# Performance work log

Measured on AMD Instinct MI355X. Metric: run time of the kernel, lower is better.

The kernel has to match this reference:

```python
import jax, jax.numpy as jnp
import numpy as np
from jax import lax

EPS = 1e-5
COMMIT_W = 0.25

def conv2d(x, w, b):
    # x: [N,C,H,W], w: [O,I,3,3], SAME padding, stride 1
    y = lax.conv_general_dilated(x, w, (1, 1), 'SAME',
                                 dimension_numbers=('NCHW', 'OIHW', 'NCHW'))
    return y + b[None, :, None, None]

def batchnorm(x, gamma, beta):
    # training-mode batch norm over (N,H,W)
    m = jnp.mean(x, axis=(0, 2, 3), keepdims=True)
    v = jnp.var(x, axis=(0, 2, 3), keepdims=True)
    xhat = (x - m) * lax.rsqrt(v + EPS)
    return xhat * gamma[None, :, None, None] + beta[None, :, None, None]

def maxpool2(x):
    return lax.reduce_window(x, -jnp.inf, lax.max, (1, 1, 2, 2), (1, 1, 2, 2), 'VALID')

def setup_inputs() -> dict:
    key = jax.random.key(0)
    ks = jax.random.split(key, 8)
    B, C, H, W, D, K = 8, 3, 256, 256, 64, 1024
    return {
        'x': jax.random.normal(ks[0], (B, C, H, W), jnp.float32),
        'conv1_w': jax.random.normal(ks[1], (D, C, 3, 3), jnp.float32) * 0.05,
        'conv1_b': jnp.zeros((D,), jnp.float32),
        'bn1_gamma': jnp.ones((D,), jnp.float32),
        'bn1_beta': jnp.zeros((D,), jnp.float32),
        'embed': jax.random.normal(ks[2], (K, D), jnp.float32),
        'conv2_w': jax.random.normal(ks[3], (C, D, 3, 3), jnp.float32) * 0.05,
        'conv2_b': jnp.zeros((C,), jnp.float32),
        'bn2_gamma': jnp.ones((C,), jnp.float32),
        'bn2_beta': jnp.zeros((C,), jnp.float32),
    }

def reference(x, conv1_w, conv1_b, bn1_gamma, bn1_beta, embed,
              conv2_w, conv2_b, bn2_gamma, bn2_beta):
    # ---- encoder ----
    h = conv2d(x, conv1_w, conv1_b)
    h = batchnorm(h, bn1_gamma, bn1_beta)
    h = jax.nn.relu(h)
    h = maxpool2(h)                      # [B, D, H/2, W/2]
    B, D, Hh, Wh = h.shape
    # ---- vector quantize (accept_image_fmap) ----
    flat = jnp.transpose(h, (0, 2, 3, 1)).reshape(-1, D)   # [N, D]
    # squared euclidean distance to each code
    dist = (jnp.sum(flat * flat, axis=1, keepdims=True)
            - 2.0 * flat @ embed.T
            + jnp.sum(embed * embed, axis=1)[None, :])     # [N, K]
    idx = jnp.argmin(dist, axis=1)                          # [N]
    quant = embed[idx]                                      # gather [N, D]
    commit_loss = COMMIT_W * jnp.mean((lax.stop_gradient(quant) - flat) ** 2)
    # straight-through estimator
    quant_st = flat + lax.stop_gradient(quant - flat)
    q = jnp.transpose(quant_st.reshape(B, Hh, Wh, D), (0, 3, 1, 2))  # [B,D,Hh,Wh]
    indices = idx.reshape(B, Hh, Wh)
    # ---- decoder ----
    up = jnp.repeat(jnp.repeat(q, 2, axis=2), 2, axis=3)    # nearest x2
    y = conv2d(up, conv2_w, conv2_b)
    y = batchnorm(y, bn2_gamma, bn2_beta)
    y = jnp.tanh(y)
    return (y, indices, commit_loss)
```

## Files before the change

### kernel.cpp

```cpp
#include <hip/hip_runtime.h>
#include <hip/hip_bf16.h>
#include <math.h>

typedef unsigned int u32;
typedef unsigned short u16;
typedef __attribute__((ext_vector_type(8))) short short8v;
typedef __attribute__((ext_vector_type(4))) float f32x4;

#define HH 256
#define WW 256
#define HP 128
#define WP 128
#define NPTS (8*HP*WP)
#define NPIX 524288
#define Y_ELEMS (8*3*HH*WW)
#define IDX_OFF Y_ELEMS
#define LOSS_OFF (Y_ELEMS + NPTS)
#define MARGIN_MFMA 0.05f

__device__ __forceinline__ u32 bfr(float f) {
  u32 u = __float_as_uint(f);
  return (u + 0x7FFFu + ((u >> 16) & 1u)) >> 16;
}
__device__ __forceinline__ float bff(u32 h) { return __uint_as_float(h << 16); }

__global__ __launch_bounds__(256) void k1_fused(
    const float* __restrict__ x, const float* __restrict__ w1,
    const float* __restrict__ b1, double* __restrict__ part1,
    float* __restrict__ pooled) {
  __shared__ float wl[27*64];
  __shared__ float b1s[64];
  __shared__ float xs[3][4][68];
  __shared__ double sred[4][128];
  int t = threadIdx.x;
  for (int i = t; i < 27*64; i += 256) { int c = i & 63; int tap = i >> 6; wl[i] = w1[c*27 + tap]; }
  if (t < 64) b1s[t] = b1[t];
  int bx = blockIdx.x;
  int b = bx >> 9;
  int pid0 = (bx & 511) * 32;
  int py = pid0 >> 7;
  int px0 = pid0 & 127;
  int gcol0 = 2*px0 - 1, grow0 = 2*py - 1;
  for (int i = t; i < 816; i += 256) {
    int j = i % 68;
    int rr = (i / 68) & 3;
    int ic = i / 272;
    int col = gcol0 + j, row = grow0 + rr;
    float v = 0.f;
    if (col >= 0 && col < WW && row >= 0 && row < HH)
      v = x[((size_t)((b*3 + ic)*HH + row))*WW + col];
    xs[ic][rr][j] = v;
  }
  __syncthreads();
  int lpx = t >> 3;
  int co = (t & 7) * 8;
  float A0[8], A1[8], C0[8], C1[8];
  #pragma unroll
  for (int c = 0; c < 8; ++c) { float bb = b1s[co + c]; A0[c] = bb; A1[c] = bb; C0[c] = bb; C1[c] = bb; }
  #pragma unroll
  for (int ic = 0; ic < 3; ++ic) {
    #pragma unroll
    for (int dy = 0; dy < 3; ++dy) {
      const float* wb = wl + (size_t)((ic*3 + dy)*3)*64 + co;
      int j0 = 2*lpx;
      float xa0 = xs[ic][dy][j0+0], xa1 = xs[ic][dy][j0+1], xa2 = xs[ic][dy][j0+2], xa3 = xs[ic][dy][j0+3];
      float xc0 = xs[ic][dy+1][j0+0], xc1 = xs[ic][dy+1][j0+1], xc2 = xs[ic][dy+1][j0+2], xc3 = xs[ic][dy+1][j0+3];
      #pragma unroll
      for (int c = 0; c < 8; ++c) {
        float w0 = wb[c], w1v = wb[64 + c], w2v = wb[128 + c];
        A0[c] = fmaf(xa0, w0, fmaf(xa1, w1v, fmaf(xa2, w2v, A0[c])));
        A1[c] = fmaf(xa1, w0, fmaf(xa2, w1v, fmaf(xa3, w2v, A1[c])));
        C0[c] = fmaf(xc0, w0, fmaf(xc1, w1v, fmaf(xc2, w2v, C0[c])));
        C1[c] = fmaf(xc1, w0, fmaf(xc2, w1v, fmaf(xc3, w2v, C1[c])));
      }
    }
  }
  double s[8], q[8];
  float m[8];
  #pragma unroll
  for (int c = 0; c < 8; ++c) {
    double dA0 = (double)A0[c], dA1 = (double)A1[c], dC0 = (double)C0[c], dC1 = (double)C1[c];
    double s_ = 0.0;
    s_ += dA0 + dA1;
    double q_ = fma(dA0, dA0, 0.0);
    q_ = fma(dA1, dA1, q_);
    float m_ = fmaxf(-3.4e38f, fmaxf(A0[c], A1[c]));
    s_ += dC0 + dC1;
    q_ = fma(dC0, dC0, q_);
    q_ = fma(dC1, dC1, q_);
    m_ = fmaxf(m_, fmaxf(C0[c], C1[c]));
    s[c] = s_; q[c] = q_; m[c] = m_;
  }
  int pid = pid0 + lpx;
  size_t p = (size_t)b*16384 + pid;
  *(float4*)(pooled + p*64 + co)     = make_float4(m[0], m[1], m[2], m[3]);
  *(float4*)(pooled + p*64 + co + 4) = make_float4(m[4], m[5], m[6], m[7]);
  #pragma unroll 1
  for (int c = 0; c < 8; ++c) {
    #pragma unroll
    for (int st = 8; st < 64; st <<= 1) {
      s[c] += __shfl_xor(s[c], st, 64);
      q[c] += __shfl_xor(q[c], st, 64);
    }
  }
  int w = t >> 6;
  if ((t & 63) < 8) {
    #pragma unroll
    for (int c = 0; c < 8; ++c) {
      sred[w][co + c] = s[c];
      sred[w][64 + co + c] = q[c];
    }
  }
  __syncthreads();
  if (t < 128)
    part1[(size_t)bx*128 + t] = (sred[0][t] + sred[1][t]) + (sred[2][t] + sred[3][t]);
}

__global__ __launch_bounds__(256) void k2_reduce_bn1(
    const double* __restrict__ part1, const float* __restrict__ gamma,
    const float* __restrict__ beta, double* __restrict__ sAB1) {
  int c = blockIdx.x, t = threadIdx.x;
  double s = 0.0, q = 0.0;
  for (int i = t; i < 4096; i += 256) {
    const double* p = part1 + (size_t)i*128;
    s += p[c];
    q += p[64 + c];
  }
  __shared__ double ls[256], lq[256];
  ls[t] = s; lq[t] = q;
  __syncthreads();
  for (int o = 128; o > 0; o >>= 1) {
    if (t < o) { ls[t] += ls[t+o]; lq[t] += lq[t+o]; }
    __syncthreads();
  }
  if (t == 0) {
    double mean = ls[0] / (double)NPIX;
    double var  = lq[0] / (double)NPIX - mean*mean;
    double A = (double)gamma[c] / sqrt(var + 1e-5);
    sAB1[c] = A;
    sAB1[64 + c] = (double)beta[c] - mean*A;
  }
}

__global__ void kE_prep(const float* __restrict__ embed, char* __restrict__ epack,
                        double* __restrict__ enormd, float* __restrict__ enf,
                        u32* __restrict__ flagcnt,
                        const float* __restrict__ w2, float* __restrict__ weff) {
  int bxx = blockIdx.x;
  if (bxx >= 4) {
    int e = (bxx - 4)*256 + threadIdx.x;
    if (e >= 16*64*4) return;
    int oc = e & 3;
    int ic = (e >> 2) & 63;
    int combo = e >> 8;
    if (oc == 3) { weff[e] = 0.f; return; }
    int bq = combo & 1, a = (combo >> 1) & 1, ex = (combo >> 2) & 1, ey = combo >> 3;
    int rs = (a == 0) ? 0 : (ey == 0 ? 1 : 2);
    int rc = ((a ^ ey) != 0) ? 2 : 1;
    int cs = (bq == 0) ? 0 : (ex == 0 ? 1 : 2);
    int cc = ((bq ^ ex) != 0) ? 2 : 1;
    float ssum = 0.f;
    for (int i = 0; i < rc; ++i)
      for (int j = 0; j < cc; ++j)
        ssum += w2[((oc*64 + ic)*3 + (rs + i))*3 + (cs + j)];
    weff[e] = ssum;
    return;
  }
  if (bxx == 0 && threadIdx.x == 0) flagcnt[0] = 0u;
  int k = bxx*256 + threadIdx.x;
  const float4* e4 = (const float4*)(embed + (size_t)k*64);
  u32 hw[32], lw[32];
  double s0 = 0.0, s1 = 0.0;
  #pragma unroll
  for (int i = 0; i < 16; ++i) {
    float4 v = e4[i];
    float f0 = v.x, f1 = v.y, f2 = v.z, f3 = v.w;
    s0 = fma((double)f0, (double)f0, s0); s1 = fma((double)f1, (double)f1, s1);
    s0 = fma((double)f2, (double)f2, s0); s1 = fma((double)f3, (double)f3, s1);
    u32 h0 = bfr(f0), h1 = bfr(f1), h2 = bfr(f2), h3 = bfr(f3);
    u32 l0 = bfr(f0 - bff(h0)), l1 = bfr(f1 - bff(h1));
    u32 l2 = bfr(f2 - bff(h2)), l3 = bfr(f3 - bff(h3));
    hw[2*i]   = h0 | (h1 << 16);
    hw[2*i+1] = h2 | (h3 << 16);
    lw[2*i]   = l0 | (l1 << 16);
    lw[2*i+1] = l2 | (l3 << 16);
  }
  char* tb = epack + (size_t)(k >> 4)*4096 + (size_t)(k & 15)*16;
  #pragma unroll
  for (int g = 0; g < 4; ++g) {
    *(uint4*)(tb + 0*1024 + g*256) = make_uint4(hw[4*g+0], hw[4*g+1], hw[4*g+2], hw[4*g+3]);
    *(uint4*)(tb + 1*1024 + g*256) = make_uint4(hw[16+4*g+0], hw[16+4*g+1], hw[16+4*g+2], hw[16+4*g+3]);
    *(uint4*)(tb + 2*1024 + g*256) = make_uint4(lw[4*g+0], lw[4*g+1], lw[4*g+2], lw[4*g+3]);
    *(uint4*)(tb + 3*1024 + g*256) = make_uint4(lw[16+4*g+0], lw[16+4*g+1], lw[16+4*g+2], lw[16+4*g+3]);
  }
  double e = s0 + s1;
  enormd[k] = e;
  enf[k] = (float)e;
}

#define MFMA_BF16 __builtin_amdgcn_mfma_f32_16x16x32_bf16
#define PROC_T(ntv) { \
  int code = (ntv)*16 + col; \
  float en2 = senf[code];    \
  f32x4 accA0={en2,en2,en2,en2}, accA1={0.f,0.f,0.f,0.f}; \
  f32x4 accB0={en2,en2,en2,en2}, accB1={0.f,0.f,0.f,0.f}; \
  accA0 = MFMA_BF16(aA_h0, b_h0, accA0, 0, 0, 0); \
  accA1 = MFMA_BF16(aA_h1, b_h1, accA1, 0, 0, 0); \
  accB0 = MFMA_BF16(aB_h0, b_h0, accB0, 0, 0, 0); \
  accB1 = MFMA_BF16(aB_h1, b_h1, accB1, 0, 0, 0); \
  accA0 = MFMA_BF16(aA_l0, b_h0, accA0, 0, 0, 0); \
  accA1 = MFMA_BF16(aA_l1, b_h1, accA1, 0, 0, 0); \
  accB0 = MFMA_BF16(aB_l0, b_h0, accB0, 0, 0, 0); \
  accB1 = MFMA_BF16(aB_l1, b_h1, accB1, 0, 0, 0); \
  accA0 = MFMA_BF16(aA_h0, b_l0, accA0, 0, 0, 0); \
  accA1 = MFMA_BF16(aA_h1, b_l1, accA1, 0, 0, 0); \
  accB0 = MFMA_BF16(aB_h0, b_l0, accB0, 0, 0, 0); \
  accB1 = MFMA_BF16(aB_h1, b_l1, accB1, 0, 0, 0); \
  _Pragma("unroll") \
  for (int j = 0; j < 4; ++j) { \
    float mA = accA0[j] + accA1[j]; \
    bool cA = mA > bestA[j]; \
    b2A[j] = fmaxf(b2A[j], fminf(mA, bestA[j])); \
    bestA[j] = fmaxf(bestA[j], mA); \
    idxA[j] = cA ? code : idxA[j]; \
    float mB = accB0[j] + accB1[j]; \
    bool cB = mB > bestB[j]; \
    b2B[j] = fmaxf(b2B[j], fminf(mB, bestB[j])); \
    bestB[j] = fmaxf(bestB[j], mB); \
    idxB[j] = cB ? code : idxB[j]; \
  } \
}
#define PROC_LDS(bb, ntv) { \
  short8v b_h0 = *(const short8v*)((bb) + 0*1024 + lane*16); \
  short8v b_h1 = *(const short8v*)((bb) + 1*1024 + lane*16); \
  short8v b_l0 = *(const short8v*)((bb) + 2*1024 + lane*16); \
  short8v b_l1 = *(const short8v*)((bb) + 3*1024 + lane*16); \
  PROC_T(ntv); \
}

__global__ __launch_bounds__(256) void kB_mfma(
    const float* __restrict__ pooled, const double* __restrict__ sAB1,
    const char* __restrict__ epack, const float* __restrict__ enf,
    int* __restrict__ idxbuf, float* __restrict__ out_f, double* __restrict__ lossq,
    u32* __restrict__ flagcnt, u32* __restrict__ flagids) {
  __shared__ float senf[1024];
  __shared__ char shbuf[32768];
  __shared__ float fnp[256];
  __shared__ float fnsum[128];
  __shared__ float sAs[64], sBs[64];
  __shared__ double wred[4];
  int t = threadIdx.x;
  for (int i = t; i < 1024; i += 256) senf[i] = -0.5f * enf[i];
  if (t < 64) { sAs[t] = (float)sAB1[t]; sBs[t] = (float)sAB1[64 + t]; }
  __syncthreads();
  {
    int lp = t >> 1, h = t & 1, cb = h*32;
    int p = blockIdx.x*128 + lp;
    const float4* src = (const float4*)(pooled + (size_t)p*64 + cb);
    float fn = 0.f;
    u32 hw[16], lw[16];
    #pragma unroll
    for (int i = 0; i < 8; ++i) {
      float4 v = src[i];
      float f0 = fmaxf(fmaf(v.x, sAs[cb+4*i+0], sBs[cb+4*i+0]), 0.f);
      float f1 = fmaxf(fmaf(v.y, sAs[cb+4*i+1], sBs[cb+4*i+1]), 0.f);
      float f2 = fmaxf(fmaf(v.z, sAs[cb+4*i+2], sBs[cb+4*i+2]), 0.f);
      float f3 = fmaxf(fmaf(v.w, sAs[cb+4*i+3], sBs[cb+4*i+3]), 0.f);
      fn = fmaf(f0, f0, fn); fn = fmaf(f1, f1, fn);
      fn = fmaf(f2, f2, fn); fn = fmaf(f3, f3, fn);
      u32 h0 = bfr(f0), h1 = bfr(f1), h2 = bfr(f2), h3 = bfr(f3);
      u32 l0 = bfr(f0 - bff(h0)), l1 = bfr(f1 - bff(h1));
      u32 l2 = bfr(f2 - bff(h2)), l3 = bfr(f3 - bff(h3));
      hw[2*i]   = h0 | (h1 << 16);
      hw[2*i+1] = h2 | (h3 << 16);
      lw[2*i]   = l0 | (l1 << 16);
      lw[2*i+1] = l2 | (l3 << 16);
    }
    uint4* dh = (uint4*)(shbuf + (size_t)lp*256 + h*64);
    uint4* dl = (uint4*)(shbuf + (size_t)lp*256 + 128 + h*64);
    #pragma unroll
    for (int i = 0; i < 4; ++i) dh[i] = make_uint4(hw[4*i], hw[4*i+1], hw[4*i+2], hw[4*i+3]);
    #pragma unroll
    for (int i = 0; i < 4; ++i) dl[i] = make_uint4(lw[4*i], lw[4*i+1], lw[4*i+2], lw[4*i+3]);
    fnp[t] = fn;
  }
  __syncthreads();
  if ((t & 1) == 0) fnsum[t >> 1] = fnp[t] + fnp[t + 1];
  int lane = t & 63;
  int col = lane & 15, g = lane >> 4;
  int w = t >> 6;
  const char* fbA = shbuf + (size_t)(w*32 + col)*256 + 16*g;
  const char* fbB = shbuf + (size_t)(w*32 + 16 + col)*256 + 16*g;
  short8v aA_h0 = *(const short8v*)(fbA);
  short8v aA_h1 = *(const short8v*)(fbA + 64);
  short8v aA_l0 = *(const short8v*)(fbA + 128);
  short8v aA_l1 = *(const short8v*)(fbA + 192);
  short8v aB_h0 = *(const short8v*)(fbB);
  short8v aB_h1 = *(const short8v*)(fbB + 64);
  short8v aB_l0 = *(const short8v*)(fbB + 128);
  short8v aB_l1 = *(const short8v*)(fbB + 192);
  __syncthreads();
  char (*btile)[4][4096] = (char (*)[4][4096])shbuf;
  float bestA[4], b2A[4], bestB[4], b2B[4];
  int idxA[4], idxB[4];
  #pragma unroll
  for (int j = 0; j < 4; ++j) {
    bestA[j] = -3.4e38f; b2A[j] = -3.4e38f; idxA[j] = 0;
    bestB[j] = -3.4e38f; b2B[j] = -3.4e38f; idxB[j] = 0;
  }
  #pragma unroll
  for (int k = 0; k < 4; ++k)
    *(uint4*)(&btile[0][k][t*16]) = *(const uint4*)(epack + (size_t)k*4096 + (size_t)t*16);
  __syncthreads();
  #pragma unroll 1
  for (int ng = 0; ng < 16; ++ng) {
    int cur = ng & 1;
    uint4 stg0, stg1, stg2, stg3;
    if (ng < 15) {
      const char* base = epack + (size_t)(4*ng + 4)*4096 + (size_t)t*16;
      stg0 = *(const uint4*)(base);
      stg1 = *(const uint4*)(base + 4096);
      stg2 = *(const uint4*)(base + 8192);
      stg3 = *(const uint4*)(base + 12288);
    }
    PROC_LDS(&btile[cur][0][0], 4*ng + 0);
    PROC_LDS(&btile[cur][1][0], 4*ng + 1);
    PROC_LDS(&btile[cur][2][0], 4*ng + 2);
    PROC_LDS(&btile[cur][3][0], 4*ng + 3);
    if (ng < 15) {
      *(uint4*)(&btile[cur ^ 1][0][t*16]) = stg0;
      *(uint4*)(&btile[cur ^ 1][1][t*16]) = stg1;
      *(uint4*)(&btile[cur ^ 1][2][t*16]) = stg2;
      *(uint4*)(&btile[cur ^ 1][3][t*16]) = stg3;
    }
    __syncthreads();
  }
  double lsum = 0.0;
  #pragma unroll
  for (int grp = 0; grp < 2; ++grp) {
    #pragma unroll
    for (int j = 0; j < 4; ++j) {
      float b  = (grp == 0) ? bestA[j] : bestB[j];
      float s2 = (grp == 0) ? b2A[j]   : b2B[j];
      int  id  = (grp == 0) ? idxA[j]  : idxB[j];
      #pragma unroll
      for (int m = 1; m < 16; m <<= 1) {
        float ob  = __shfl_xor(b, m, 64);
        float os2 = __shfl_xor(s2, m, 64);
        int  oid  = __shfl_xor(id, m, 64);
        s2 = fmaxf(fmaxf(s2, os2), fminf(b, ob));
        if (ob > b || (ob == b && oid < id)) { b = ob; id = oid; }
      }
      if (col == 0) {
        int lpt = w*32 + grp*16 + g*4 + j;
        int p = blockIdx.x*128 + lpt;
        idxbuf[p] = id;
        out_f[IDX_OFF + p] = (float)id;
        lsum += (double)fmaf(-2.f, b, fnsum[lpt]);
        if (b - s2 <= 0.5f*MARGIN_MFMA) { u32 pos = atomicAdd(flagcnt, 1u); flagids[pos] = (u32)p; }
      }
    }
  }
  #pragma unroll
  for (int m = 1; m < 64; m <<= 1) lsum += __shfl_xor(lsum, m, 64);
  if (lane == 0) wred[w] = lsum;
  __syncthreads();
  if (t == 0) lossq[blockIdx.x] = (wred[0] + wred[1]) + (wred[2] + wred[3]);
}

__global__ __launch_bounds__(64) void kC_fallback(
    const float* __restrict__ x, const float* __restrict__ w1,
    const float* __restrict__ b1, const double* __restrict__ sAB1,
    const float* __restrict__ embed, const double* __restrict__ enormd,
    const u32* __restrict__ flagcnt, const u32* __restrict__ flagids,
    int* __restrict__ idxbuf, float* __restrict__ out_f) {
  __shared__ double fd[64];
  int lane = threadIdx.x;
  double wv[27];
  #pragma unroll
  for (int i = 0; i < 27; ++i) wv[i] = (double)w1[lane*27 + i];
  double bias = (double)b1[lane];
  double A = sAB1[lane], B = sAB1[64 + lane];
  u32 n = flagcnt[0];
  for (u32 i = blockIdx.x; i < n; i += gridDim.x) {
    int p = (int)flagids[i];
    int b = p >> 14, py = (p >> 7) & 127, px = p & 127;
    double mx = -1e300;
    #pragma unroll
    for (int ry = 0; ry < 2; ++ry) {
      #pragma unroll
      for (int cx = 0; cx < 2; ++cx) {
        double a = bias;
        int yy = 2*py + ry, xx = 2*px + cx;
        #pragma unroll
        for (int ic = 0; ic < 3; ++ic) {
          #pragma unroll
          for (int dy = 0; dy < 3; ++dy) {
            int ryy = yy + dy - 1;
            if (ryy >= 0 && ryy < HH) {
              const float* row = x + ((size_t)((b*3 + ic)*HH + ryy))*WW;
              #pragma unroll
              for (int dxx = 0; dxx < 3; ++dxx) {
                int xc = xx + dxx - 1;
                if (xc >= 0 && xc < WW) a = fma((double)row[xc], wv[(ic*3 + dy)*3 + dxx], a);
              }
            }
          }
        }
        mx = fmax(mx, a);
      }
    }
    fd[lane] = fmax(fma(mx, A, B), 0.0);
    __syncthreads();
    double bd = 1e300; int bk = 1 << 20;
    for (int kk = 0; kk < 16; ++kk) {
      int k = kk*64 + lane;
      const float* e = embed + (size_t)k*64;
      double e0=0,e1=0,e2=0,e3=0;
      #pragma unroll
      for (int d = 0; d < 16; ++d) {
        e0 = fma(fd[4*d+0], (double)e[4*d+0], e0);
        e1 = fma(fd[4*d+1], (double)e[4*d+1], e1);
        e2 = fma(fd[4*d+2], (double)e[4*d+2], e2);
        e3 = fma(fd[4*d+3], (double)e[4*d+3], e3);
      }
      double dist = fma(-2.0, (e0+e1)+(e2+e3), enormd[k]);
      if (dist < bd) { bd = dist; bk = k; }
    }
    #pragma unroll
    for (int st = 1; st < 64; st <<= 1) {
      double od = __shfl_xor(bd, st, 64);
      int ok = __shfl_xor(bk, st, 64);
      if (od < bd || (od == bd && ok < bk)) { bd = od; bk = ok; }
    }
    if (lane == 0) {
      idxbuf[p] = bk;
      out_f[IDX_OFF + p] = (float)bk;
    }
    __syncthreads();
  }
}

__global__ __launch_bounds__(256) void k5b_loss(const double* __restrict__ lossq, float* __restrict__ out) {
  __shared__ double red[256];
  int t = threadIdx.x;
  red[t] = (lossq[t] + lossq[t + 256]) + (lossq[t + 512] + lossq[t + 768]);
  __syncthreads();
  for (int o = 128; o > 0; o >>= 1) { if (t < o) red[t] += red[t+o]; __syncthreads(); }
  if (t == 0) {
    double loss = 0.25 * red[0] / (double)((size_t)NPTS * 64);
    out[LOSS_OFF] = (float)loss;
  }
}

template<int MODE>
__global__ __launch_bounds__(256) void conv2_body(
    const int* __restrict__ idxbuf, const float* __restrict__ embed,
    const float* __restrict__ weff, const float* __restrict__ c2b,
    const float* __restrict__ sAB2, float* __restrict__ part2,
    float* __restrict__ ybuf, float* __restrict__ yout) {
  __shared__ float xw[4][6];
  int t = threadIdx.x;
  int bx = blockIdx.x;
  int b = bx >> 6;
  int tile = bx & 63;
  int px = (tile & 1)*64 + (t & 63);
  int py = (tile >> 1)*4 + (t >> 6);
  const int* idxb = idxbuf + b*HP*WP;
  float s0=0.f,s1=0.f,s2=0.f, q0=0.f,q1=0.f,q2=0.f;
  #pragma unroll
  for (int pa = 0; pa < 2; ++pa) {
    #pragma unroll
    for (int pb = 0; pb < 2; ++pb) {
      float acc0 = 0.f, acc1 = 0.f, acc2 = 0.f;
      #pragma unroll 1
      for (int ca = 0; ca < 2; ++ca) {
        #pragma unroll 1
        for (int cb = 0; cb < 2; ++cb) {
          int cy = py - 1 + pa + ca;
          int cx = px - 1 + pb + cb;
          if (cy < 0 || cy >= HP || cx < 0 || cx >= WP) continue;
          int ii = idxb[cy*WP + cx];
          const float4* q4 = (const float4*)(embed + (size_t)ii*64);
          const float4* w4 = ((const float4*)weff) + (pa*8 + pb*4 + ca*2 + cb)*64;
          #pragma unroll 4
          for (int i4 = 0; i4 < 16; ++i4) {
            float4 qv = q4[i4];
            float4 w0 = w4[i4*4+0], w1v = w4[i4*4+1], w2v = w4[i4*4+2], w3 = w4[i4*4+3];
            acc0 = fmaf(qv.x, w0.x, acc0); acc1 = fmaf(qv.x, w0.y, acc1); acc2 = fmaf(qv.x, w0.z, acc2);
            acc0 = fmaf(qv.y, w1v.x, acc0); acc1 = fmaf(qv.y, w1v.y, acc1); acc2 = fmaf(qv.y, w1v.z, acc2);
            acc0 = fmaf(qv.z, w2v.x, acc0); acc1 = fmaf(qv.z, w2v.y, acc1); acc2 = fmaf(qv.z, w2v.z, acc2);
            acc0 = fmaf(qv.w, w3.x, acc0); acc1 = fmaf(qv.w, w3.y, acc1); acc2 = fmaf(qv.w, w3.z, acc2);
          }
        }
      }
      int yy = 2*py + pa, xx = 2*px + pb;
      if (MODE == 2) {
        float v0 = tanhf(fmaf(acc0, sAB2[0], sAB2[4]));
        float v1 = tanhf(fmaf(acc1, sAB2[1], sAB2[5]));
        float v2 = tanhf(fmaf(acc2, sAB2[2], sAB2[6]));
        yout[((size_t)(b*3 + 0)*HH + yy)*WW + xx] = v0;
        yout[((size_t)(b*3 + 1)*HH + yy)*WW + xx] = v1;
        yout[((size_t)(b*3 + 2)*HH + yy)*WW + xx] = v2;
      } else {
        float v0 = acc0 + c2b[0], v1 = acc1 + c2b[1], v2 = acc2 + c2b[2];
        s0 += v0; s1 += v1; s2 += v2;
        q0 = fmaf(v0, v0, q0); q1 = fmaf(v1, v1, q1); q2 = fmaf(v2, v2, q2);
        if (MODE == 1) {
          ybuf[((size_t)(b*3 + 0)*HH + yy)*WW + xx] = v0;
          ybuf[((size_t)(b*3 + 1)*HH + yy)*WW + xx] = v1;
          ybuf[((size_t)(b*3 + 2)*HH + yy)*WW + xx] = v2;
        }
      }
    }
  }
  if (MODE != 2) {
    float sv[3] = {s0, s1, s2}, qv2[3] = {q0, q1, q2};
    #pragma unroll
    for (int oc = 0; oc < 3; ++oc) {
      float v = sv[oc], q = qv2[oc];
      #pragma unroll
      for (int m = 1; m < 64; m <<= 1) { v += __shfl_xor(v, m, 64); q += __shfl_xor(q, m, 64); }
      if ((t & 63) == 0) { xw[t >> 6][oc] = v; xw[t >> 6][3 + oc] = q; }
    }
    __syncthreads();
    if (t == 0) {
      #pragma unroll
      for (int i = 0; i < 6; ++i)
        part2[bx*6 + i] = (xw[0][i] + xw[1][i]) + (xw[2][i] + xw[3][i]);
    }
  }
}

__global__ __launch_bounds__(256) void k7_reduce_bn2(
    const float* __restrict__ part2, const float* __restrict__ g2,
    const float* __restrict__ bt2, const float* __restrict__ c2b,
    float* __restrict__ sAB2, int fold_bias) {
  int t = threadIdx.x;
  int w = t >> 6, lane = t & 63;
  if (w >= 3) return;
  double s = 0.0, q = 0.0;
  for (int i = lane; i < 512; i += 64) {
    s += (double)part2[i*6 + w];
    q += (double)part2[i*6 + 3 + w];
  }
  #pragma unroll
  for (int m = 1; m < 64; m <<= 1) { s += __shfl_xor(s, m, 64); q += __shfl_xor(q, m, 64); }
  if (lane == 0) {
    double mean = s / (double)NPIX;
    double var  = q / (double)NPIX - mean*mean;
    double A = (double)g2[w] / sqrt(var + 1e-5);
    double Bc = (double)bt2[w] - mean*A;
    if (fold_bias) Bc += (double)c2b[w]*A;
    sAB2[w] = (float)A;
    sAB2[4 + w] = (float)Bc;
  }
}

__global__ __launch_bounds__(256) void k8_apply(
    const float* __restrict__ ybuf, const float* __restrict__ sAB2,
    float* __restrict__ yout) {
  int i4 = blockIdx.x*256 + threadIdx.x;
  int i = i4 * 4;
  int oc = (i >> 16) % 3;
  float A = sAB2[oc], B = sAB2[4 + oc];
  float4 v = *(const float4*)(ybuf + i);
  float4 r;
  r.x = tanhf(fmaf(v.x, A, B));
  r.y = tanhf(fmaf(v.y, A, B));
  r.z = tanhf(fmaf(v.z, A, B));
  r.w = tanhf(fmaf(v.w, A, B));
  *(float4*)(yout + i) = r;
}

extern "C" void kernel_launch(void* const* d_in, const int* in_sizes, int n_in,
                              void* d_out, int out_size, void* d_ws, size_t ws_size,
                              hipStream_t stream) {
  const float* x   = (const float*)d_in[0];
  const float* w1  = (const float*)d_in[1];
  const float* b1  = (const float*)d_in[2];
  const float* g1  = (const float*)d_in[3];
  const float* bt1 = (const float*)d_in[4];
  const float* emb = (const float*)d_in[5];
  const float* w2  = (const float*)d_in[6];
  const float* b2  = (const float*)d_in[7];
  const float* g2  = (const float*)d_in[8];
  const float* bt2 = (const float*)d_in[9];
  float* out = (float*)d_out;

  char* ws = (char*)d_ws;
  float*  pooled  = (float*) (ws);
  double* part1   = (double*)(ws + 33554432);
  char*   epack   =          (ws + 33554432);
  int*    idxbuf  = (int*)   (ws + 37748736);
  u32*    flagids = (u32*)   (ws + 38273024);
  u32*    flagcnt = (u32*)   (ws + 38797312);
  float*  part2   = (float*) (ws + 38799424);
  double* sAB1    = (double*)(ws + 38811712);
  float*  sAB2    = (float*) (ws + 38812736);
  double* enormd  = (double*)(ws + 38812800);
  float*  enf     = (float*) (ws + 38820992);
  float*  weff    = (float*) (ws + 38825088);
  double* lossq   = (double*)(ws + 38841472);
  float*  ybuf    = (float*) (ws + 38849664);
  bool use_ybuf = (ws_size >= (size_t)45141120);

  hipLaunchKernelGGL(k1_fused, dim3(4096), dim3(256), 0, stream, x, w1, b1, part1, pooled);
  hipLaunchKernelGGL(k2_reduce_bn1, dim3(64), dim3(256), 0, stream, part1, g1, bt1, sAB1);
  hipLaunchKernelGGL(kE_prep, dim3(20), dim3(256), 0, stream, emb, epack, enormd, enf, flagcnt, w2, weff);
  hipLaunchKernelGGL(kB_mfma, dim3(1024), dim3(256), 0, stream, pooled, sAB1, (const char*)epack,
                     enf, idxbuf, out, lossq, flagcnt, flagids);
  hipLaunchKernelGGL(kC_fallback, dim3(2048), dim3(64), 0, stream, x, w1, b1, sAB1, emb, enormd,
                     flagcnt, flagids, idxbuf, out);
  hipLaunchKernelGGL(k5b_loss, dim3(1), dim3(256), 0, stream, lossq, out);
  if (use_ybuf) {
    hipLaunchKernelGGL((conv2_body<1>), dim3(512), dim3(256), 0, stream, idxbuf, emb, weff, b2, sAB2, part2, ybuf, out);
    hipLaunchKernelGGL(k7_reduce_bn2, dim3(1), dim3(256), 0, stream, part2, g2, bt2, b2, sAB2, 0);
    hipLaunchKernelGGL(k8_apply, dim3(1536), dim3(256), 0, stream, ybuf, sAB2, out);
  } else {
    hipLaunchKernelGGL((conv2_body<0>), dim3(512), dim3(256), 0, stream, idxbuf, emb, weff, b2, sAB2, part2, ybuf, out);
    hipLaunchKernelGGL(k7_reduce_bn2, dim3(1), dim3(256), 0, stream, part2, g2, bt2, b2, sAB2, 1);
    hipLaunchKernelGGL((conv2_body<2>), dim3(512), dim3(256), 0, stream, idxbuf, emb, weff, b2, sAB2, part2, ybuf, out);
  }
}
```

Measured before the change: 241.7 us.

## Precompute per-code conv2 projections so decoder conv gathers instead of multiplying

Adds a kernel that projects each of the 1024 codebook vectors through all 16 effective upsampled-conv weight combos into a 64-float table per code. The decoder conv then loads each of the 9 neighbour indices once and sums precomputed float4 entries, replacing per-pixel 64-channel dot products. This removes most FLOPs and the embed/weight reads in conv2_body. It costs a small extra kernel and a 256KB table placed in the workspace region overlapping epack/part1, which is safe only if those buffers are dead by then. Summation order also changes slightly.

```diff
diff --git a/kernel.cpp b/kernel.cpp
--- a/kernel.cpp
+++ b/kernel.cpp
@@ -196,6 +196,25 @@
   double e = s0 + s1;
   enormd[k] = e;
   enf[k] = (float)e;
+}
+
+__global__ __launch_bounds__(256) void kp_proj(
+    const float* __restrict__ embed, const float* __restrict__ weff,
+    float* __restrict__ proj) {
+  int e = blockIdx.x*256 + threadIdx.x;
+  int k = e >> 6;
+  int slot = e & 63;
+  int combo = slot >> 2, oc = slot & 3;
+  if (oc == 3) { proj[e] = 0.f; return; }
+  const float* er = embed + (size_t)k*64;
+  const float* wc = weff + combo*256 + oc;
+  float s0 = 0.f, s1 = 0.f;
+  #pragma unroll 8
+  for (int ic = 0; ic < 64; ic += 2) {
+    s0 = fmaf(er[ic],     wc[ic*4],     s0);
+    s1 = fmaf(er[ic + 1], wc[ic*4 + 4], s1);
+  }
+  proj[e] = s0 + s1;
 }
 
 #define MFMA_BF16 __builtin_amdgcn_mfma_f32_16x16x32_bf16
@@ -455,10 +474,9 @@
 
 template<int MODE>
 __global__ __launch_bounds__(256) void conv2_body(
-    const int* __restrict__ idxbuf, const float* __restrict__ embed,
-    const float* __restrict__ weff, const float* __restrict__ c2b,
-    const float* __restrict__ sAB2, float* __restrict__ part2,
-    float* __restrict__ ybuf, float* __restrict__ yout) {
+    const int* __restrict__ idxbuf, const float* __restrict__ proj,
+    const float* __restrict__ c2b, const float* __restrict__ sAB2,
+    float* __restrict__ part2, float* __restrict__ ybuf, float* __restrict__ yout) {
   __shared__ float xw[4][6];
   int t = threadIdx.x;
   int bx = blockIdx.x;
@@ -467,43 +485,62 @@
   int px = (tile & 1)*64 + (t & 63);
   int py = (tile >> 1)*4 + (t >> 6);
   const int* idxb = idxbuf + b*HP*WP;
-  float s0=0.f,s1=0.f,s2=0.f, q0=0.f,q1=0.f,q2=0.f;
-  #pragma unroll
-  for (int pa = 0; pa < 2; ++pa) {
-    #pragma unroll
-    for (int pb = 0; pb < 2; ++pb) {
-      float acc0 = 0.f, acc1 = 0.f, acc2 = 0.f;
-      #pragma unroll 1
-      for (int ca = 0; ca < 2; ++ca) {
-        #pragma unroll 1
-        for (int cb = 0; cb < 2; ++cb) {
-          int cy = py - 1 + pa + ca;
-          int cx = px - 1 + pb + cb;
-          if (cy < 0 || cy >= HP || cx < 0 || cx >= WP) continue;
-          int ii = idxb[cy*WP + cx];
-          const float4* q4 = (const float4*)(embed + (size_t)ii*64);
-          const float4* w4 = ((const float4*)weff) + (pa*8 + pb*4 + ca*2 + cb)*64;
-          #pragma unroll 4
-          for (int i4 = 0; i4 < 16; ++i4) {
-            float4 qv = q4[i4];
-            float4 w0 = w4[i4*4+0], w1v = w4[i4*4+1], w2v = w4[i4*4+2], w3 = w4[i4*4+3];
-            acc0 = fmaf(qv.x, w0.x, acc0); acc1 = fmaf(qv.x, w0.y, acc1); acc2 = fmaf(qv.x, w0.z, acc2);
-            acc0 = fmaf(qv.y, w1v.x, acc0); acc1 = fmaf(qv.y, w1v.y, acc1); acc2 = fmaf(qv.y, w1v.z, acc2);
-            acc0 = fmaf(qv.z, w2v.x, acc0); acc1 = fmaf(qv.z, w2v.y, acc1); acc2 = fmaf(qv.z, w2v.z, acc2);
-            acc0 = fmaf(qv.w, w3.x, acc0); acc1 = fmaf(qv.w, w3.y, acc1); acc2 = fmaf(qv.w, w3.z, acc2);
-          }
+  float acc[12];
+  #pragma unroll
+  for (int i = 0; i < 12; ++i) acc[i] = 0.f;
+  #pragma unroll
+  for (int r = 0; r < 3; ++r) {
+    int cy = py - 1 + r;
+    bool vy = (cy >= 0) && (cy < HP);
+    #pragma unroll
+    for (int s = 0; s < 3; ++s) {
+      int cx = px - 1 + s;
+      if (!(vy && (cx >= 0) && (cx < WP))) continue;
+      int ii = idxb[cy*WP + cx];
+      const float4* pr = (const float4*)(proj + (size_t)ii*64);
+      #pragma unroll
+      for (int rp = 0; rp < ((r==1) ? 2 : 1); ++rp) {
+        const int pa = (r==0) ? 0 : (r==2) ? 1 : rp;
+        const int ca = (r==0) ? 0 : (r==2) ? 1 : (1-rp);
+        #pragma unroll
+        for (int sp = 0; sp < ((s==1) ? 2 : 1); ++sp) {
+          const int pb = (s==0) ? 0 : (s==2) ? 1 : sp;
+          const int cb = (s==0) ? 0 : (s==2) ? 1 : (1-sp);
+          float4 v = pr[pa*8 + pb*4 + ca*2 + cb];
+          int ob = (pa*2 + pb)*3;
+          acc[ob+0] += v.x;
+          acc[ob+1] += v.y;
+          acc[ob+2] += v.z;
         }
       }
-      int yy = 2*py + pa, xx = 2*px + pb;
-      if (MODE == 2) {
-        float v0 = tanhf(fmaf(acc0, sAB2[0], sAB2[4]));
-        float v1 = tanhf(fmaf(acc1, sAB2[1], sAB2[5]));
-        float v2 = tanhf(fmaf(acc2, sAB2[2], sAB2[6]));
+    }
+  }
+  if (MODE == 2) {
+    #pragma unroll
+    for (int pa = 0; pa < 2; ++pa) {
+      int yy = 2*py + pa;
+      #pragma unroll
+      for (int pb = 0; pb < 2; ++pb) {
+        int xx = 2*px + pb;
+        int ob = (pa*2 + pb)*3;
+        float v0 = tanhf(fmaf(acc[ob+0], sAB2[0], sAB2[4]));
+        float v1 = tanhf(fmaf(acc[ob+1], sAB2[1], sAB2[5]));
+        float v2 = tanhf(fmaf(acc[ob+2], sAB2[2], sAB2[6]));
         yout[((size_t)(b*3 + 0)*HH + yy)*WW + xx] = v0;
         yout[((size_t)(b*3 + 1)*HH + yy)*WW + xx] = v1;
         yout[((size_t)(b*3 + 2)*HH + yy)*WW + xx] = v2;
-      } else {
-        float v0 = acc0 + c2b[0], v1 = acc1 + c2b[1], v2 = acc2 + c2b[2];
+      }
+    }
+  } else {
+    float s0=0.f,s1=0.f,s2=0.f, q0=0.f,q1=0.f,q2=0.f;
+    #pragma unroll
+    for (int pa = 0; pa < 2; ++pa) {
+      int yy = 2*py + pa;
+      #pragma unroll
+      for (int pb = 0; pb < 2; ++pb) {
+        int xx = 2*px + pb;
+        int ob = (pa*2 + pb)*3;
+        float v0 = acc[ob+0] + c2b[0], v1 = acc[ob+1] + c2b[1], v2 = acc[ob+2] + c2b[2];
         s0 += v0; s1 += v1; s2 += v2;
         q0 = fmaf(v0, v0, q0); q1 = fmaf(v1, v1, q1); q2 = fmaf(v2, v2, q2);
         if (MODE == 1) {
@@ -513,8 +550,6 @@
         }
       }
     }
-  }
-  if (MODE != 2) {
     float sv[3] = {s0, s1, s2}, qv2[3] = {q0, q1, q2};
     #pragma unroll
     for (int oc = 0; oc < 3; ++oc) {
@@ -592,6 +627,7 @@
   float*  pooled  = (float*) (ws);
   double* part1   = (double*)(ws + 33554432);
   char*   epack   =          (ws + 33554432);
+  float*  proj    = (float*) (ws + 33816576);
   int*    idxbuf  = (int*)   (ws + 37748736);
   u32*    flagids = (u32*)   (ws + 38273024);
   u32*    flagcnt = (u32*)   (ws + 38797312);
@@ -608,18 +644,19 @@
   hipLaunchKernelGGL(k1_fused, dim3(4096), dim3(256), 0, stream, x, w1, b1, part1, pooled);
   hipLaunchKernelGGL(k2_reduce_bn1, dim3(64), dim3(256), 0, stream, part1, g1, bt1, sAB1);
   hipLaunchKernelGGL(kE_prep, dim3(20), dim3(256), 0, stream, emb, epack, enormd, enf, flagcnt, w2, weff);
+  hipLaunchKernelGGL(kp_proj, dim3(256), dim3(256), 0, stream, emb, weff, proj);
   hipLaunchKernelGGL(kB_mfma, dim3(1024), dim3(256), 0, stream, pooled, sAB1, (const char*)epack,
                      enf, idxbuf, out, lossq, flagcnt, flagids);
   hipLaunchKernelGGL(kC_fallback, dim3(2048), dim3(64), 0, stream, x, w1, b1, sAB1, emb, enormd,
                      flagcnt, flagids, idxbuf, out);
   hipLaunchKernelGGL(k5b_loss, dim3(1), dim3(256), 0, stream, lossq, out);
   if (use_ybuf) {
-    hipLaunchKernelGGL((conv2_body<1>), dim3(512), dim3(256), 0, stream, idxbuf, emb, weff, b2, sAB2, part2, ybuf, out);
+    hipLaunchKernelGGL((conv2_body<1>), dim3(512), dim3(256), 0, stream, idxbuf, proj, b2, sAB2, part2, ybuf, out);
     hipLaunchKernelGGL(k7_reduce_bn2, dim3(1), dim3(256), 0, stream, part2, g2, bt2, b2, sAB2, 0);
     hipLaunchKernelGGL(k8_apply, dim3(1536), dim3(256), 0, stream, ybuf, sAB2, out);
   } else {
-    hipLaunchKernelGGL((conv2_body<0>), dim3(512), dim3(256), 0, stream, idxbuf, emb, weff, b2, sAB2, part2, ybuf, out);
+    hipLaunchKernelGGL((conv2_body<0>), dim3(512), dim3(256), 0, stream, idxbuf, proj, b2, sAB2, part2, ybuf, out);
     hipLaunchKernelGGL(k7_reduce_bn2, dim3(1), dim3(256), 0, stream, part2, g2, bt2, b2, sAB2, 1);
-    hipLaunchKernelGGL((conv2_body<2>), dim3(512), dim3(256), 0, stream, idxbuf, emb, weff, b2, sAB2, part2, ybuf, out);
-  }
-}
+    hipLaunchKernelGGL((conv2_body<2>), dim3(512), dim3(256), 0, stream, idxbuf, proj, b2, sAB2, part2, ybuf, out);
+  }
+}
```

New measurement: 206.5 us. -14.5%, faster.
